# Performance work log

Measured on AMD Instinct MI355X. Metric: run time of the kernel, lower is better.

The kernel has to match this reference:

```python
import jax, jax.numpy as jnp
import numpy as np

B, T, S1, S2 = 64, 256, 256, 256
E = 512   # tgt_word_vec_size
D = 512   # decoder_rnn_size
NT_V, RULE_V = 600, 50000


def _attention(q, ctx, mask, Wa, Wo):
    # OpenNMT GlobalAttention, attn_type='general', no bias.
    # q: [B, D], ctx: [B, S, D], mask: [B, S] bool
    scores = jnp.einsum('bd,bsd->bs', q @ Wa, ctx)
    scores = jnp.where(mask, scores, jnp.float32(-1e9))
    a = jax.nn.softmax(scores, axis=-1)
    c = jnp.einsum('bs,bsd->bd', a, ctx)
    out = jnp.tanh(jnp.concatenate([c, q], axis=-1) @ Wo)
    return out, a


def _lstm_cell(x, h, c, Wih, Whh, b):
    g = x @ Wih.T + h @ Whh.T + b
    i, f, gg, o = jnp.split(g, 4, axis=-1)  # torch gate order i,f,g,o
    c2 = jax.nn.sigmoid(f) * c + jax.nn.sigmoid(i) * jnp.tanh(gg)
    h2 = jax.nn.sigmoid(o) * jnp.tanh(c2)
    return h2, c2


def setup_inputs() -> dict:
    key = jax.random.key(0)
    ks = jax.random.split(key, 20)
    s = 0.02
    inp = {
        'nt': jax.random.randint(ks[0], (B, T), 0, NT_V, dtype=jnp.int32),
        'prev_rules': jax.random.randint(ks[1], (B, T), 0, RULE_V, dtype=jnp.int32),
        'parent_rules': jax.random.randint(ks[2], (B, T), 0, RULE_V, dtype=jnp.int32),
        'parent_idx': jax.random.randint(ks[3], (B, T), 0, T, dtype=jnp.int32),
        'src_context': jax.random.normal(ks[4], (B, S1, D), jnp.float32),
        'rest_context': jax.random.normal(ks[5], (B, S2, D), jnp.float32),
        'src_mask': jnp.ones((B, S1), dtype=bool),
        'rest_mask': jnp.ones((B, S2), dtype=bool),
        'h0': jax.random.normal(ks[6], (B, D), jnp.float32),
        'c0': jax.random.normal(ks[7], (B, D), jnp.float32),
        'nt_emb': jax.random.normal(ks[8], (NT_V, E), jnp.float32) * s,
        'rule_emb': jax.random.normal(ks[9], (RULE_V, E), jnp.float32) * s,
        'Wih': jax.random.normal(ks[10], (4 * D, 3 * E + D), jnp.float32) * s,
        'Whh': jax.random.normal(ks[11], (4 * D, D), jnp.float32) * s,
        'b_lstm': jnp.zeros((4 * D,), jnp.float32),
        'Wa_src': jax.random.normal(ks[12], (D, D), jnp.float32) * s,
        'Wo_src': jax.random.normal(ks[13], (2 * D, D), jnp.float32) * s,
        'Wa_var': jax.random.normal(ks[14], (D, D), jnp.float32) * s,
        'Wo_var': jax.random.normal(ks[15], (2 * D, D), jnp.float32) * s,
        'Wl': jax.random.normal(ks[16], (3 * D, D), jnp.float32) * s,
        'bl': jnp.zeros((D,), jnp.float32),
    }
    return inp


def reference(nt, prev_rules, parent_rules, parent_idx, src_context, rest_context,
              src_mask, rest_mask, h0, c0, nt_emb, rule_emb, Wih, Whh, b_lstm,
              Wa_src, Wo_src, Wa_var, Wo_var, Wl, bl):
    b, t = nt.shape
    d = h0.shape[-1]
    nt_e = nt_emb[nt]              # [B,T,E]
    rule_e = rule_emb[prev_rules]  # [B,T,E]
    prule_e = rule_emb[parent_rules]
    buf0 = jnp.zeros((b, t, d), src_context.dtype)  # rnn_output buffer (tree parent states)

    def step(carry, xs):
        h, c, buf = carry
        nt_t, r_t, pr_t, pidx_t, ti = xs
        # parent state: earlier rnn_output per batch element (zeros if not yet written)
        parent = jnp.take_along_axis(buf, pidx_t[:, None, None], axis=1)[:, 0]  # [B,D]
        x = jnp.concatenate([nt_t, r_t, pr_t, parent], axis=-1)
        h, c = _lstm_cell(x, h, c, Wih, Whh, b_lstm)
        src_out, _ = _attention(h, src_context, src_mask, Wa_src, Wo_src)
        var_out, var_sc = _attention(src_out, rest_context, rest_mask, Wa_var, Wo_var)
        ao = jnp.tanh(jnp.concatenate([h, src_out, var_out], axis=-1) @ Wl + bl)
        buf = jax.lax.dynamic_update_slice_in_dim(buf, h[:, None, :], ti, axis=1)
        return (h, c, buf), (ao, var_sc)

    xs = (nt_e.transpose(1, 0, 2), rule_e.transpose(1, 0, 2), prule_e.transpose(1, 0, 2),
          parent_idx.T, jnp.arange(t))
    _, (outs, scores) = jax.lax.scan(step, (h0, c0, buf0), xs)
    output = outs.transpose(1, 0, 2)       # [B,T,D]
    attn_scores = scores.transpose(1, 0, 2)  # [B,T,S2]
    # forward returns (output, attn_scores, copy_attn_scores); copy == var scores
    return output, attn_scores, attn_scores
```

## Files before the change

kernel.cpp:

```cpp
#include <hip/hip_runtime.h>
#include <hip/hip_bf16.h>
#include <math.h>

typedef __bf16 bf16;
typedef float  f32x4  __attribute__((ext_vector_type(4)));
typedef bf16   bf16x8 __attribute__((ext_vector_type(8)));
typedef bf16   bf16x4 __attribute__((ext_vector_type(4)));
typedef unsigned long long u64;

#define NB 64
#define NT 256
#define NS 256
#define ND 512

__device__ __forceinline__ f32x4 mfma16(bf16x8 a, bf16x8 b, f32x4 c) {
  return __builtin_amdgcn_mfma_f32_16x16x32_bf16(a, b, c, 0, 0, 0);
}

__global__ void k_cast_bt(bf16* dst, int dstStride, int N, int K,
                          const float* src, int srcLd, int srcOff, int transpose) {
  int id = blockIdx.x * 256 + threadIdx.x;
  if (id >= N * K) return;
  int n = id / K, k = id % K;
  float v = transpose ? src[(size_t)k * srcLd + srcOff + n]
                      : src[(size_t)n * srcLd + srcOff + k];
  dst[(size_t)n * dstStride + k] = (bf16)v;
}

__global__ void k_init(const float* h0, bf16* h0bf, unsigned* bar) {
  int id = blockIdx.x * 256 + threadIdx.x;
  if (id < NB * ND) h0bf[id] = (bf16)h0[id];
  if (id == 0) *bar = 0u;
}

__global__ void k_embed(const int* __restrict__ nt, const int* __restrict__ pr,
                        const int* __restrict__ par, const float* __restrict__ nt_emb,
                        const float* __restrict__ rule_emb, bf16* __restrict__ Abuf) {
  int r = blockIdx.x;
  int tid = threadIdx.x;
  const float* s0 = nt_emb  + (size_t)nt[r]  * 512;
  const float* s1 = rule_emb + (size_t)pr[r]  * 512;
  const float* s2 = rule_emb + (size_t)par[r] * 512;
  bf16* drow = Abuf + (size_t)r * 1536;
  for (int v = 0; v < 3; ++v) {
    int col = (tid + v * 128) * 4;
    const float* s = (col < 512) ? (s0 + col) : (col < 1024 ? s1 + col - 512 : s2 + col - 1024);
    float4 x = *(const float4*)s;
    bf16x4 y; y[0] = (bf16)x.x; y[1] = (bf16)x.y; y[2] = (bf16)x.z; y[3] = (bf16)x.w;
    *(bf16x4*)(drow + col) = y;
  }
}

__global__ __launch_bounds__(256) void k_gemm(
    const bf16* __restrict__ A0, int k0, const bf16* __restrict__ A1, int k1,
    const bf16* __restrict__ A2, int k2, const bf16* __restrict__ Bt,
    int Ktot, int N, int nbx, const float* __restrict__ bias, int act,
    float* __restrict__ Cf, bf16* __restrict__ Cbf) {
  __shared__ bf16 Al[128 * 40];
  __shared__ bf16 Bl[128 * 40];
  const int tid = threadIdx.x;
  const int bx = blockIdx.x % nbx, by = blockIdx.x / nbx;
  const int w = tid >> 6, l = tid & 63;
  const int wm = (w & 1) * 64, wn = (w >> 1) * 64;
  const int la = l & 15, kq = (l >> 4) * 8;
  const int srow = tid >> 1, skh = (tid & 1) * 16;
  const int m_g = by * 128 + srow;
  const bf16* brow = Bt + (size_t)(bx * 128 + srow) * Ktot;

  f32x4 acc[4][4];
  f32x4 z; z[0] = 0.f; z[1] = 0.f; z[2] = 0.f; z[3] = 0.f;
#pragma unroll
  for (int mt = 0; mt < 4; ++mt)
#pragma unroll
    for (int nt2 = 0; nt2 < 4; ++nt2) acc[mt][nt2] = z;

  for (int kt = 0; kt < Ktot; kt += 32) {
    __syncthreads();
    {
      int kg = kt + skh;
      const bf16* p;
      int kk = kg;
      if (kk < k0) p = A0 + (size_t)m_g * k0 + kk;
      else { kk -= k0;
        if (kk < k1) p = A1 + (size_t)m_g * k1 + kk;
        else { kk -= k1; p = A2 + (size_t)m_g * k2 + kk; } }
      *(bf16x8*)(&Al[srow * 40 + skh])     = *(const bf16x8*)p;
      *(bf16x8*)(&Al[srow * 40 + skh + 8]) = *(const bf16x8*)(p + 8);
      const bf16* q = brow + kt + skh;
      *(bf16x8*)(&Bl[srow * 40 + skh])     = *(const bf16x8*)q;
      *(bf16x8*)(&Bl[srow * 40 + skh + 8]) = *(const bf16x8*)(q + 8);
    }
    __syncthreads();
    bf16x8 af[4], bfr[4];
#pragma unroll
    for (int mt = 0; mt < 4; ++mt) af[mt]  = *(const bf16x8*)(&Al[(wm + mt * 16 + la) * 40 + kq]);
#pragma unroll
    for (int nt2 = 0; nt2 < 4; ++nt2) bfr[nt2] = *(const bf16x8*)(&Bl[(wn + nt2 * 16 + la) * 40 + kq]);
#pragma unroll
    for (int mt = 0; mt < 4; ++mt)
#pragma unroll
      for (int nt2 = 0; nt2 < 4; ++nt2)
        acc[mt][nt2] = mfma16(af[mt], bfr[nt2], acc[mt][nt2]);
  }
  const int r4 = (l >> 4) * 4, cc = l & 15;
#pragma unroll
  for (int mt = 0; mt < 4; ++mt)
#pragma unroll
    for (int nt2 = 0; nt2 < 4; ++nt2)
#pragma unroll
      for (int i = 0; i < 4; ++i) {
        int mm = by * 128 + wm + mt * 16 + r4 + i;
        int nn = bx * 128 + wn + nt2 * 16 + cc;
        float v = acc[mt][nt2][i];
        if (bias) v += bias[nn];
        if (act) v = tanhf(v);
        size_t off = (size_t)mm * N + nn;
        if (Cf)  Cf[off]  = v;
        if (Cbf) Cbf[off] = (bf16)v;
      }
}

__global__ __launch_bounds__(512, 2) void k_lstm_all(
    const bf16* __restrict__ gpre, const bf16* __restrict__ W2bt,
    const int* __restrict__ parent_idx, const bf16* __restrict__ h0bf,
    const float* __restrict__ c0,
    bf16* __restrict__ Hbf, float* __restrict__ H, unsigned* __restrict__ bar) {
  __shared__ bf16 Als[2][64 * 72];
  __shared__ float gls[64 * 68];
  const int tid = threadIdx.x;
  const int bid = blockIdx.x;
  const int d0 = bid * 16;
  const int w = tid >> 6, l = tid & 63;
  const int wm = (w & 1) * 32;
  const int wn = (w >> 1) * 16;
  const int la16 = l & 15, kq8 = (l >> 4) * 8, r4 = (l >> 4) * 4;
  const int am = tid >> 3;
  const int akoff = (tid & 7) * 8;
  const int pb = tid >> 3, pd = (tid & 7) * 2;

  const int ng = (wn >> 4) * 512 + d0 + la16;
  bf16x8 wf[32];
#pragma unroll
  for (int kc = 0; kc < 32; ++kc)
    wf[kc] = *(const bf16x8*)(W2bt + (size_t)ng * 1024 + kc * 32 + kq8);

  float creg0 = c0[pb * ND + d0 + pd];
  float creg1 = c0[pb * ND + d0 + pd + 1];

  unsigned g_pf[4];
#pragma unroll
  for (int g = 0; g < 4; ++g)
    g_pf[g] = *(const unsigned*)(gpre + ((size_t)pb * NT + 0) * 2048 + g * 512 + d0 + pd);

  for (int t = 0; t < NT; ++t) {
    const int pidx_v = parent_idx[am * NT + t];
    const bool haspar = (pidx_v < t);
    const bf16* hsrc = (t == 0) ? (h0bf + (size_t)am * ND)
                                : (Hbf + ((size_t)am * NT + (t - 1)) * ND);
    const bf16* psrc = Hbf + ((size_t)am * NT + pidx_v) * ND;

    auto issueA = [&](int it, u64& x0, u64& x1) {
      if (it < 8) {
        const bf16* p = hsrc + it * 64 + akoff;
        x0 = __hip_atomic_load((const u64*)p,       __ATOMIC_RELAXED, __HIP_MEMORY_SCOPE_AGENT);
        x1 = __hip_atomic_load((const u64*)(p + 4), __ATOMIC_RELAXED, __HIP_MEMORY_SCOPE_AGENT);
      } else if (haspar) {
        const bf16* p = psrc + (it - 8) * 64 + akoff;
        x0 = __hip_atomic_load((const u64*)p,       __ATOMIC_RELAXED, __HIP_MEMORY_SCOPE_AGENT);
        x1 = __hip_atomic_load((const u64*)(p + 4), __ATOMIC_RELAXED, __HIP_MEMORY_SCOPE_AGENT);
      } else { x0 = 0ull; x1 = 0ull; }
    };
    auto wrA = [&](int buf, u64 x0, u64 x1) {
      *(u64*)(&Als[buf][am * 72 + akoff])     = x0;
      *(u64*)(&Als[buf][am * 72 + akoff + 4]) = x1;
    };

    u64 s0a, s0b, s1a, s1b;
    issueA(0, s0a, s0b);
    issueA(1, s1a, s1b);
    wrA(0, s0a, s0b);
    issueA(2, s0a, s0b);
    __syncthreads();

    f32x4 acc[2];
    f32x4 zf; zf[0] = 0.f; zf[1] = 0.f; zf[2] = 0.f; zf[3] = 0.f;
    acc[0] = zf; acc[1] = zf;

#pragma unroll
    for (int it = 0; it < 16; ++it) {
      const int cur = it & 1, nxt = cur ^ 1;
      if (it < 15) {
        if (nxt) { wrA(1, s1a, s1b); if (it + 3 < 16) issueA(it + 3, s1a, s1b); }
        else     { wrA(0, s0a, s0b); if (it + 3 < 16) issueA(it + 3, s0a, s0b); }
      }
      const bf16* base = Als[cur];
      bf16x8 af[2][2];
#pragma unroll
      for (int mt = 0; mt < 2; ++mt)
#pragma unroll
        for (int kh = 0; kh < 2; ++kh)
          af[mt][kh] = *(const bf16x8*)(base + (wm + mt * 16 + la16) * 72 + kh * 32 + kq8);
#pragma unroll
      for (int mt = 0; mt < 2; ++mt)
#pragma unroll
        for (int kh = 0; kh < 2; ++kh)
          acc[mt] = mfma16(af[mt][kh], wf[2 * it + kh], acc[mt]);
      __syncthreads();
    }

#pragma unroll
    for (int mt = 0; mt < 2; ++mt)
#pragma unroll
      for (int i = 0; i < 4; ++i)
        gls[(wm + mt * 16 + r4 + i) * 68 + wn + la16] = acc[mt][i];
    __syncthreads();

    {
      union { unsigned u; bf16 h[2]; } gv[4];
#pragma unroll
      for (int g = 0; g < 4; ++g) gv[g].u = g_pf[g];
      float hn[2];
#pragma unroll
      for (int j = 0; j < 2; ++j) {
        float gi = gls[pb * 68 +  0 + pd + j] + (float)gv[0].h[j];
        float gf = gls[pb * 68 + 16 + pd + j] + (float)gv[1].h[j];
        float gg = gls[pb * 68 + 32 + pd + j] + (float)gv[2].h[j];
        float go = gls[pb * 68 + 48 + pd + j] + (float)gv[3].h[j];
        float si = 1.f / (1.f + __expf(-gi));
        float sf = 1.f / (1.f + __expf(-gf));
        float so = 1.f / (1.f + __expf(-go));
        float cp = j ? creg1 : creg0;
        float cn = sf * cp + si * tanhf(gg);
        if (j) creg1 = cn; else creg0 = cn;
        hn[j] = so * tanhf(cn);
      }
      size_t hoff = ((size_t)pb * NT + t) * ND + d0 + pd;
      union { unsigned u; bf16 h[2]; } pk;
      pk.h[0] = (bf16)hn[0]; pk.h[1] = (bf16)hn[1];
      __hip_atomic_store((unsigned*)(Hbf + hoff), pk.u, __ATOMIC_RELAXED, __HIP_MEMORY_SCOPE_AGENT);
      *(float2*)(H + hoff) = make_float2(hn[0], hn[1]);
    }

    if (t + 1 < NT) {
#pragma unroll
      for (int g = 0; g < 4; ++g)
        g_pf[g] = *(const unsigned*)(gpre + ((size_t)pb * NT + (t + 1)) * 2048 + g * 512 + d0 + pd);
      __syncthreads();
      if (tid == 0) {
        __hip_atomic_fetch_add(bar, 1u, __ATOMIC_RELAXED, __HIP_MEMORY_SCOPE_AGENT);
        const unsigned target = 32u * (unsigned)(t + 1);
        while (__hip_atomic_load(bar, __ATOMIC_RELAXED, __HIP_MEMORY_SCOPE_AGENT) < target)
          __builtin_amdgcn_s_sleep(1);
      }
      __syncthreads();
    }
  }
}

__global__ __launch_bounds__(256) void k_gemm_f32(
    const float* __restrict__ A, const float* __restrict__ Bm, float* __restrict__ C,
    int M, int N, int K, int nbx) {
  __shared__ float At[16 * 68];
  __shared__ float Bs[16 * 68];
  const int tid = threadIdx.x;
  const int bx = blockIdx.x % nbx, by = blockIdx.x / nbx;
  const int ty = tid >> 4, tx = tid & 15;
  const int am = tid >> 2, ak = (tid & 3) * 4;
  const int bk = tid >> 4, bn = (tid & 15) * 4;
  float acc[4][4] = {};
  for (int kb = 0; kb < K; kb += 16) {
    __syncthreads();
    float4 a4 = *(const float4*)(A + (size_t)(by * 64 + am) * K + kb + ak);
    At[(ak + 0) * 68 + am] = a4.x; At[(ak + 1) * 68 + am] = a4.y;
    At[(ak + 2) * 68 + am] = a4.z; At[(ak + 3) * 68 + am] = a4.w;
    *(float4*)(&Bs[bk * 68 + bn]) = *(const float4*)(Bm + (size_t)(kb + bk) * N + bx * 64 + bn);
    __syncthreads();
#pragma unroll
    for (int kk = 0; kk < 16; ++kk) {
      float4 av = *(const float4*)(&At[kk * 68 + ty * 4]);
      float4 bv = *(const float4*)(&Bs[kk * 68 + tx * 4]);
      float aa[4] = {av.x, av.y, av.z, av.w};
      float bb[4] = {bv.x, bv.y, bv.z, bv.w};
#pragma unroll
      for (int i = 0; i < 4; ++i)
#pragma unroll
        for (int j = 0; j < 4; ++j) acc[i][j] += aa[i] * bb[j];
    }
  }
#pragma unroll
  for (int i = 0; i < 4; ++i) {
    float4 o; o.x = acc[i][0]; o.y = acc[i][1]; o.z = acc[i][2]; o.w = acc[i][3];
    *(float4*)(C + (size_t)(by * 64 + ty * 4 + i) * N + bx * 64 + tx * 4) = o;
  }
}

__global__ __launch_bounds__(256) void k_attn(
    const float* __restrict__ Q, const float* __restrict__ ctx, bf16* __restrict__ Cbf,
    float* __restrict__ prob0, float* __restrict__ prob1) {
  __shared__ float Sl[64 * 257];
  __shared__ float T1[16 * 68];
  __shared__ float T2[16 * 68];
  const int tid = threadIdx.x;
  const int b = blockIdx.x >> 2, ch = blockIdx.x & 3;
  const int t0 = ch * 64;
  const int row0 = b * NT + t0;
  const int ty = tid >> 4, tx = tid & 15;
  const int sl_r = tid >> 2, sl_k = (tid & 3) * 4;

  for (int sc = 0; sc < 4; ++sc) {
    float acc[4][4] = {};
    for (int kc = 0; kc < 512; kc += 16) {
      __syncthreads();
      float4 q4 = *(const float4*)(Q + (size_t)(row0 + sl_r) * ND + kc + sl_k);
      T1[(sl_k + 0) * 68 + sl_r] = q4.x; T1[(sl_k + 1) * 68 + sl_r] = q4.y;
      T1[(sl_k + 2) * 68 + sl_r] = q4.z; T1[(sl_k + 3) * 68 + sl_r] = q4.w;
      float4 c4 = *(const float4*)(ctx + (size_t)(b * NS + sc * 64 + sl_r) * ND + kc + sl_k);
      T2[(sl_k + 0) * 68 + sl_r] = c4.x; T2[(sl_k + 1) * 68 + sl_r] = c4.y;
      T2[(sl_k + 2) * 68 + sl_r] = c4.z; T2[(sl_k + 3) * 68 + sl_r] = c4.w;
      __syncthreads();
#pragma unroll
      for (int kk = 0; kk < 16; ++kk) {
        float4 qv = *(const float4*)(&T1[kk * 68 + ty * 4]);
        float4 cv = *(const float4*)(&T2[kk * 68 + tx * 4]);
        float qa[4] = {qv.x, qv.y, qv.z, qv.w};
        float ca[4] = {cv.x, cv.y, cv.z, cv.w};
#pragma unroll
        for (int i = 0; i < 4; ++i)
#pragma unroll
          for (int j = 0; j < 4; ++j) acc[i][j] += qa[i] * ca[j];
      }
    }
#pragma unroll
    for (int i = 0; i < 4; ++i)
#pragma unroll
      for (int j = 0; j < 4; ++j)
        Sl[(ty * 4 + i) * 257 + sc * 64 + tx * 4 + j] = acc[i][j];
  }
  __syncthreads();

  if (tid < 64) {
    float* row = &Sl[tid * 257];
    float mx = -1e30f;
    for (int s = 0; s < 256; ++s) mx = fmaxf(mx, row[s]);
    float sum = 0.f;
    for (int s = 0; s < 256; ++s) { float e = __expf(row[s] - mx); row[s] = e; sum += e; }
    float inv = 1.f / sum;
    for (int s = 0; s < 256; ++s) row[s] *= inv;
  }
  __syncthreads();
  if (prob0) {
    int pr = tid >> 2, pq = (tid & 3) * 64;
    size_t po = (size_t)(row0 + pr) * NS + pq;
    for (int s = 0; s < 64; s += 4) {
      float4 o; o.x = Sl[pr * 257 + pq + s];     o.y = Sl[pr * 257 + pq + s + 1];
      o.z = Sl[pr * 257 + pq + s + 2];           o.w = Sl[pr * 257 + pq + s + 3];
      *(float4*)(prob0 + po + s) = o;
      *(float4*)(prob1 + po + s) = o;
    }
  }

  const int c_sr = tid >> 4, c_n4 = (tid & 15) * 4;
  for (int dc = 0; dc < 512; dc += 64) {
    float acc[4][4] = {};
    for (int s0c = 0; s0c < 256; s0c += 16) {
      __syncthreads();
      *(float4*)(&T2[c_sr * 68 + c_n4]) =
          *(const float4*)(ctx + (size_t)(b * NS + s0c + c_sr) * ND + dc + c_n4);
      __syncthreads();
#pragma unroll
      for (int kk = 0; kk < 16; ++kk) {
        float p0 = Sl[(ty * 4 + 0) * 257 + s0c + kk];
        float p1 = Sl[(ty * 4 + 1) * 257 + s0c + kk];
        float p2 = Sl[(ty * 4 + 2) * 257 + s0c + kk];
        float p3 = Sl[(ty * 4 + 3) * 257 + s0c + kk];
        float4 cv = *(const float4*)(&T2[kk * 68 + tx * 4]);
        float ca[4] = {cv.x, cv.y, cv.z, cv.w};
#pragma unroll
        for (int j = 0; j < 4; ++j) {
          acc[0][j] += p0 * ca[j]; acc[1][j] += p1 * ca[j];
          acc[2][j] += p2 * ca[j]; acc[3][j] += p3 * ca[j];
        }
      }
    }
#pragma unroll
    for (int i = 0; i < 4; ++i)
#pragma unroll
      for (int j = 0; j < 4; ++j)
        Cbf[(size_t)(row0 + ty * 4 + i) * ND + dc + tx * 4 + j] = (bf16)acc[i][j];
  }
}

extern "C" void kernel_launch(void* const* d_in, const int* in_sizes, int n_in,
                              void* d_out, int out_size, void* d_ws, size_t ws_size,
                              hipStream_t stream) {
  const int*   nt       = (const int*)d_in[0];
  const int*   prules   = (const int*)d_in[1];
  const int*   parules  = (const int*)d_in[2];
  const int*   pidx     = (const int*)d_in[3];
  const float* src_ctx  = (const float*)d_in[4];
  const float* rest_ctx = (const float*)d_in[5];
  const float* h0       = (const float*)d_in[8];
  const float* c0       = (const float*)d_in[9];
  const float* nt_emb   = (const float*)d_in[10];
  const float* rule_emb = (const float*)d_in[11];
  const float* Wih      = (const float*)d_in[12];
  const float* Whh      = (const float*)d_in[13];
  const float* b_lstm   = (const float*)d_in[14];
  const float* Wa_src   = (const float*)d_in[15];
  const float* Wo_src   = (const float*)d_in[16];
  const float* Wa_var   = (const float*)d_in[17];
  const float* Wo_var   = (const float*)d_in[18];
  const float* Wl       = (const float*)d_in[19];
  const float* bl       = (const float*)d_in[20];
  float* out = (float*)d_out;

  char* p = (char*)d_ws;
  bf16*  Abuf    = (bf16*)p;  p += 50331648;
  bf16*  gpre    = (bf16*)p;  p += 67108864;
  float* H       = (float*)p; p += 33554432;
  bf16*  Hbf     = (bf16*)p;  p += 16777216;
  float* SRCOUT  = (float*)p; p += 33554432;
  bf16*  SRCOUTb = (bf16*)p;  p += 16777216;
  bf16*  Wemb_bt = (bf16*)p;  p += 6291456;
  bf16*  W2bt    = (bf16*)p;  p += 4194304;
  bf16*  Wos_bt  = (bf16*)p;  p += 1048576;
  bf16*  Wov_bt  = (bf16*)p;  p += 1048576;
  bf16*  Wl_bt   = (bf16*)p;  p += 1572864;
  bf16*  h0bf    = (bf16*)p;  p += 65536;
  unsigned* bar  = (unsigned*)p; p += 256;
  float* Q1    = (float*)Abuf;
  bf16*  C1bf  = (bf16*)((char*)Abuf + 33554432);
  float* Q2    = (float*)gpre;
  bf16*  C2bf  = (bf16*)((char*)gpre + 33554432);
  bf16*  VARbf = (bf16*)((char*)gpre + 50331648);
  float* out_p0 = out + 8388608;
  float* out_p1 = out + 12582912;

  k_cast_bt<<<(2048*1536+255)/256, 256, 0, stream>>>(Wemb_bt, 1536, 2048, 1536, Wih, 2048, 0, 0);
  k_cast_bt<<<(2048*512 +255)/256, 256, 0, stream>>>(W2bt,        1024, 2048, 512, Whh, 512, 0, 0);
  k_cast_bt<<<(2048*512 +255)/256, 256, 0, stream>>>(W2bt + 512,  1024, 2048, 512, Wih, 2048, 1536, 0);
  k_cast_bt<<<(512*1024 +255)/256, 256, 0, stream>>>(Wos_bt, 1024, 512, 1024, Wo_src, 512, 0, 1);
  k_cast_bt<<<(512*1024 +255)/256, 256, 0, stream>>>(Wov_bt, 1024, 512, 1024, Wo_var, 512, 0, 1);
  k_cast_bt<<<(512*1536 +255)/256, 256, 0, stream>>>(Wl_bt,  1536, 512, 1536, Wl, 512, 0, 1);
  k_init<<<128, 256, 0, stream>>>(h0, h0bf, bar);
  k_embed<<<16384, 128, 0, stream>>>(nt, prules, parules, nt_emb, rule_emb, Abuf);

  k_gemm<<<2048, 256, 0, stream>>>(Abuf, 1536, nullptr, 0, nullptr, 0,
                                   Wemb_bt, 1536, 2048, 16, b_lstm, 0, nullptr, gpre);

  k_lstm_all<<<32, 512, 0, stream>>>(gpre, W2bt, pidx, h0bf, c0, Hbf, H, bar);

  k_gemm_f32<<<2048, 256, 0, stream>>>(H, Wa_src, Q1, 16384, 512, 512, 8);
  k_attn<<<256, 256, 0, stream>>>(Q1, src_ctx, C1bf, nullptr, nullptr);
  k_gemm<<<512, 256, 0, stream>>>(C1bf, 512, Hbf, 512, nullptr, 0,
                                  Wos_bt, 1024, 512, 4, nullptr, 1, SRCOUT, SRCOUTb);
  k_gemm_f32<<<2048, 256, 0, stream>>>(SRCOUT, Wa_var, Q2, 16384, 512, 512, 8);
  k_attn<<<256, 256, 0, stream>>>(Q2, rest_ctx, C2bf, out_p0, out_p1);
  k_gemm<<<512, 256, 0, stream>>>(C2bf, 512, SRCOUTb, 512, nullptr, 0,
                                  Wov_bt, 1024, 512, 4, nullptr, 1, nullptr, VARbf);
  k_gemm<<<512, 256, 0, stream>>>(Hbf, 512, SRCOUTb, 512, VARbf, 512,
                                  Wl_bt, 1536, 512, 4, bl, 1, out, nullptr);
}
```

Baseline: 3.168 ms.

## Restructure persistent LSTM recurrence with split-batch blocks, flag barrier and early parent GEMM

The recurrent LSTM kernel now runs 64 blocks, each handling half the batch for 16 hidden units. Warps are split so half compute the h-part of the recurrent GEMM with 32x32 MFMAs while the other half prefetch the parent state and compute the parent contribution ahead of the grid barrier, unless a parent is the just-produced step, in which case it is deferred. The single atomic counter barrier is replaced by per-block flags polled by one wavefront. Hidden states are also written to a time-major buffer so the next step loads them contiguously into LDS. This aims to shorten the serial per-step critical path, at the cost of more LDS, a second store per step, and more complex synchronisation.

```diff
diff --git a/kernel.cpp b/kernel.cpp
--- a/kernel.cpp
+++ b/kernel.cpp
@@ -4,6 +4,7 @@
 
 typedef __bf16 bf16;
 typedef float  f32x4  __attribute__((ext_vector_type(4)));
+typedef float  f32x16 __attribute__((ext_vector_type(16)));
 typedef bf16   bf16x8 __attribute__((ext_vector_type(8)));
 typedef bf16   bf16x4 __attribute__((ext_vector_type(4)));
 typedef unsigned long long u64;
@@ -15,6 +16,9 @@
 
 __device__ __forceinline__ f32x4 mfma16(bf16x8 a, bf16x8 b, f32x4 c) {
   return __builtin_amdgcn_mfma_f32_16x16x32_bf16(a, b, c, 0, 0, 0);
+}
+__device__ __forceinline__ f32x16 mfma32(bf16x8 a, bf16x8 b, f32x16 c) {
+  return __builtin_amdgcn_mfma_f32_32x32x16_bf16(a, b, c, 0, 0, 0);
 }
 
 __global__ void k_cast_bt(bf16* dst, int dstStride, int N, int K,
@@ -30,7 +34,7 @@
 __global__ void k_init(const float* h0, bf16* h0bf, unsigned* bar) {
   int id = blockIdx.x * 256 + threadIdx.x;
   if (id < NB * ND) h0bf[id] = (bf16)h0[id];
-  if (id == 0) *bar = 0u;
+  if (id < 1024) bar[id] = 0u;
 }
 
 __global__ void k_embed(const int* __restrict__ nt, const int* __restrict__ pr,
@@ -120,140 +124,194 @@
       }
 }
 
+#define LSTM_LDS 100992
+
 __global__ __launch_bounds__(512, 2) void k_lstm_all(
     const bf16* __restrict__ gpre, const bf16* __restrict__ W2bt,
     const int* __restrict__ parent_idx, const bf16* __restrict__ h0bf,
     const float* __restrict__ c0,
-    bf16* __restrict__ Hbf, float* __restrict__ H, unsigned* __restrict__ bar) {
-  __shared__ bf16 Als[2][64 * 72];
-  __shared__ float gls[64 * 68];
+    bf16* __restrict__ Hbf,
+    bf16* __restrict__ Ht,
+    float* __restrict__ H, unsigned* __restrict__ flags) {
+  extern __shared__ char smem[];
+  bf16*  Als      = (bf16*)smem;
+  float* gls      = (float*)(smem + 66048);
+  unsigned* latew = (unsigned*)(smem + 100864);
+
   const int tid = threadIdx.x;
   const int bid = blockIdx.x;
-  const int d0 = bid * 16;
+  const int bg = bid & 1, cg = bid >> 1;
+  const int d0 = cg * 16;
   const int w = tid >> 6, l = tid & 63;
-  const int wm = (w & 1) * 32;
-  const int wn = (w >> 1) * 16;
-  const int la16 = l & 15, kq8 = (l >> 4) * 8, r4 = (l >> 4) * 4;
-  const int am = tid >> 3;
-  const int akoff = (tid & 7) * 8;
-  const int pb = tid >> 3, pd = (tid & 7) * 2;
-
-  const int ng = (wn >> 4) * 512 + d0 + la16;
-  bf16x8 wf[32];
-#pragma unroll
-  for (int kc = 0; kc < 32; ++kc)
-    wf[kc] = *(const bf16x8*)(W2bt + (size_t)ng * 1024 + kc * 32 + kq8);
-
-  float creg0 = c0[pb * ND + d0 + pd];
-  float creg1 = c0[pb * ND + d0 + pd + 1];
-
+  const int la32 = l & 31, lhi = l >> 5, kq8 = lhi * 8;
+  const int n2 = w & 1, kq = w >> 1;
+  const int lc = n2 * 32 + la32;
+  const int ng = (lc >> 4) * 512 + d0 + (lc & 15);
+
+  bf16x8 wf[16];
+#pragma unroll
+  for (int kc = 0; kc < 16; ++kc)
+    wf[kc] = *(const bf16x8*)(W2bt + (size_t)ng * 1024 + kq * 256 + kc * 16 + kq8);
+
+  const int pb = (tid & 255) >> 3;
+  const int pdh = (tid & 7) * 2;
+  const int gb = bg * 32 + pb;
+  const int ss = tid & 255, pr = ss & 31, po = ss >> 5;
+  const int pgb = bg * 32 + pr;
+
+  float creg0 = 0.f, creg1 = 0.f;
   unsigned g_pf[4];
-#pragma unroll
-  for (int g = 0; g < 4; ++g)
-    g_pf[g] = *(const unsigned*)(gpre + ((size_t)pb * NT + 0) * 2048 + g * 512 + d0 + pd);
+  if (tid < 256) {
+    creg0 = c0[(size_t)gb * ND + d0 + pdh];
+    creg1 = c0[(size_t)gb * ND + d0 + pdh + 1];
+#pragma unroll
+    for (int g = 0; g < 4; ++g)
+      g_pf[g] = *(const unsigned*)(gpre + ((size_t)gb * NT) * 2048 + g * 512 + d0 + pdh);
+  }
+
+  if (w < 4) {
+    const bf16* src = h0bf + (size_t)bg * 32 * ND;
+#pragma unroll
+    for (int j = 0; j < 16; ++j) {
+      u64 x = *(const u64*)(src + w * 4096 + j * 256 + l * 4);
+      *(u64*)(&Als[(w * 8 + (j >> 1)) * 1032 + (j & 1) * 256 + l * 4]) = x;
+    }
+  }
+  f32x16 acc;
+#pragma unroll
+  for (int i = 0; i < 16; ++i) acc[i] = 0.f;
+  bool deferred = false;
+  __syncthreads();
 
   for (int t = 0; t < NT; ++t) {
-    const int pidx_v = parent_idx[am * NT + t];
-    const bool haspar = (pidx_v < t);
-    const bf16* hsrc = (t == 0) ? (h0bf + (size_t)am * ND)
-                                : (Hbf + ((size_t)am * NT + (t - 1)) * ND);
-    const bf16* psrc = Hbf + ((size_t)am * NT + pidx_v) * ND;
-
-    auto issueA = [&](int it, u64& x0, u64& x1) {
-      if (it < 8) {
-        const bf16* p = hsrc + it * 64 + akoff;
-        x0 = __hip_atomic_load((const u64*)p,       __ATOMIC_RELAXED, __HIP_MEMORY_SCOPE_AGENT);
-        x1 = __hip_atomic_load((const u64*)(p + 4), __ATOMIC_RELAXED, __HIP_MEMORY_SCOPE_AGENT);
-      } else if (haspar) {
-        const bf16* p = psrc + (it - 8) * 64 + akoff;
-        x0 = __hip_atomic_load((const u64*)p,       __ATOMIC_RELAXED, __HIP_MEMORY_SCOPE_AGENT);
-        x1 = __hip_atomic_load((const u64*)(p + 4), __ATOMIC_RELAXED, __HIP_MEMORY_SCOPE_AGENT);
-      } else { x0 = 0ull; x1 = 0ull; }
-    };
-    auto wrA = [&](int buf, u64 x0, u64 x1) {
-      *(u64*)(&Als[buf][am * 72 + akoff])     = x0;
-      *(u64*)(&Als[buf][am * 72 + akoff + 4]) = x1;
-    };
-
-    u64 s0a, s0b, s1a, s1b;
-    issueA(0, s0a, s0b);
-    issueA(1, s1a, s1b);
-    wrA(0, s0a, s0b);
-    issueA(2, s0a, s0b);
-    __syncthreads();
-
-    f32x4 acc[2];
-    f32x4 zf; zf[0] = 0.f; zf[1] = 0.f; zf[2] = 0.f; zf[3] = 0.f;
-    acc[0] = zf; acc[1] = zf;
-
-#pragma unroll
-    for (int it = 0; it < 16; ++it) {
-      const int cur = it & 1, nxt = cur ^ 1;
-      if (it < 15) {
-        if (nxt) { wrA(1, s1a, s1b); if (it + 3 < 16) issueA(it + 3, s1a, s1b); }
-        else     { wrA(0, s0a, s0b); if (it + 3 < 16) issueA(it + 3, s0a, s0b); }
-      }
-      const bf16* base = Als[cur];
-      bf16x8 af[2][2];
-#pragma unroll
-      for (int mt = 0; mt < 2; ++mt)
-#pragma unroll
-        for (int kh = 0; kh < 2; ++kh)
-          af[mt][kh] = *(const bf16x8*)(base + (wm + mt * 16 + la16) * 72 + kh * 32 + kq8);
-#pragma unroll
-      for (int mt = 0; mt < 2; ++mt)
-#pragma unroll
-        for (int kh = 0; kh < 2; ++kh)
-          acc[mt] = mfma16(af[mt][kh], wf[2 * it + kh], acc[mt]);
-      __syncthreads();
-    }
-
-#pragma unroll
-    for (int mt = 0; mt < 2; ++mt)
-#pragma unroll
-      for (int i = 0; i < 4; ++i)
-        gls[(wm + mt * 16 + r4 + i) * 68 + wn + la16] = acc[mt][i];
-    __syncthreads();
-
-    {
+    u64 preg[16];
+    if (w < 4) {
+#pragma unroll
+      for (int kc = 0; kc < 16; ++kc) {
+        bf16x8 a = *(const bf16x8*)(&Als[la32 * 1032 + kq * 256 + kc * 16 + kq8]);
+        acc = mfma32(a, wf[kc], acc);
+      }
+    } else {
+      if (deferred) {
+#pragma unroll
+        for (int kc = 0; kc < 16; ++kc) {
+          bf16x8 a = *(const bf16x8*)(&Als[la32 * 1032 + kq * 256 + kc * 16 + kq8]);
+          acc = mfma32(a, wf[kc], acc);
+        }
+      }
+      if (t + 1 < NT) {
+        int pv = parent_idx[(size_t)pgb * NT + t + 1];
+        if (pv < t) {
+          const bf16* p = Hbf + ((size_t)pgb * NT + pv) * ND + po * 64;
+#pragma unroll
+          for (int j = 0; j < 16; ++j)
+            preg[j] = __hip_atomic_load((const u64*)(p + j * 4),
+                                        __ATOMIC_RELAXED, __HIP_MEMORY_SCOPE_AGENT);
+        } else {
+#pragma unroll
+          for (int j = 0; j < 16; ++j) preg[j] = 0ull;
+        }
+      }
+    }
+#pragma unroll
+    for (int i = 0; i < 16; ++i) {
+      int row = (i & 3) + 8 * (i >> 2) + 4 * lhi;
+      gls[(kq * 32 + row) * 68 + lc] = acc[i];
+    }
+#pragma unroll
+    for (int i = 0; i < 16; ++i) acc[i] = 0.f;
+    __syncthreads();
+
+    if (tid < 256) {
       union { unsigned u; bf16 h[2]; } gv[4];
 #pragma unroll
       for (int g = 0; g < 4; ++g) gv[g].u = g_pf[g];
       float hn[2];
 #pragma unroll
       for (int j = 0; j < 2; ++j) {
-        float gi = gls[pb * 68 +  0 + pd + j] + (float)gv[0].h[j];
-        float gf = gls[pb * 68 + 16 + pd + j] + (float)gv[1].h[j];
-        float gg = gls[pb * 68 + 32 + pd + j] + (float)gv[2].h[j];
-        float go = gls[pb * 68 + 48 + pd + j] + (float)gv[3].h[j];
-        float si = 1.f / (1.f + __expf(-gi));
-        float sf = 1.f / (1.f + __expf(-gf));
-        float so = 1.f / (1.f + __expf(-go));
+        float s[4];
+#pragma unroll
+        for (int g = 0; g < 4; ++g) {
+          float v = 0.f;
+#pragma unroll
+          for (int q = 0; q < 4; ++q) v += gls[(q * 32 + pb) * 68 + g * 16 + pdh + j];
+          s[g] = v + (float)gv[g].h[j];
+        }
+        float si = 1.f / (1.f + __expf(-s[0]));
+        float sf = 1.f / (1.f + __expf(-s[1]));
+        float so = 1.f / (1.f + __expf(-s[3]));
+        float e2 = __expf(2.f * fminf(fmaxf(s[2], -15.f), 15.f));
+        float tg = (e2 - 1.f) / (e2 + 1.f);
         float cp = j ? creg1 : creg0;
-        float cn = sf * cp + si * tanhf(gg);
+        float cn = sf * cp + si * tg;
+        float e2c = __expf(2.f * fminf(fmaxf(cn, -15.f), 15.f));
+        float tc = (e2c - 1.f) / (e2c + 1.f);
         if (j) creg1 = cn; else creg0 = cn;
-        hn[j] = so * tanhf(cn);
-      }
-      size_t hoff = ((size_t)pb * NT + t) * ND + d0 + pd;
+        hn[j] = so * tc;
+      }
       union { unsigned u; bf16 h[2]; } pk;
       pk.h[0] = (bf16)hn[0]; pk.h[1] = (bf16)hn[1];
-      __hip_atomic_store((unsigned*)(Hbf + hoff), pk.u, __ATOMIC_RELAXED, __HIP_MEMORY_SCOPE_AGENT);
-      *(float2*)(H + hoff) = make_float2(hn[0], hn[1]);
-    }
-
-    if (t + 1 < NT) {
-#pragma unroll
-      for (int g = 0; g < 4; ++g)
-        g_pf[g] = *(const unsigned*)(gpre + ((size_t)pb * NT + (t + 1)) * 2048 + g * 512 + d0 + pd);
-      __syncthreads();
-      if (tid == 0) {
-        __hip_atomic_fetch_add(bar, 1u, __ATOMIC_RELAXED, __HIP_MEMORY_SCOPE_AGENT);
-        const unsigned target = 32u * (unsigned)(t + 1);
-        while (__hip_atomic_load(bar, __ATOMIC_RELAXED, __HIP_MEMORY_SCOPE_AGENT) < target)
-          __builtin_amdgcn_s_sleep(1);
-      }
-      __syncthreads();
-    }
+      size_t hb = ((size_t)gb * NT + t) * ND + d0 + pdh;
+      size_t ho = ((size_t)t * NB + gb) * ND + d0 + pdh;
+      __hip_atomic_store((unsigned*)(Hbf + hb), pk.u, __ATOMIC_RELAXED, __HIP_MEMORY_SCOPE_AGENT);
+      __hip_atomic_store((unsigned*)(Ht + ho), pk.u, __ATOMIC_RELAXED, __HIP_MEMORY_SCOPE_AGENT);
+      *(float2*)(H + hb) = make_float2(hn[0], hn[1]);
+      if (t + 1 < NT) {
+#pragma unroll
+        for (int g = 0; g < 4; ++g)
+          g_pf[g] = *(const unsigned*)(gpre + ((size_t)gb * NT + t + 1) * 2048 + g * 512 + d0 + pdh);
+      }
+    }
+
+    bool deferred_next = false;
+    if (w >= 4 && t + 1 < NT) {
+#pragma unroll
+      for (int j = 0; j < 16; ++j)
+        *(u64*)(&Als[pr * 1032 + 512 + po * 64 + j * 4]) = preg[j];
+      int pv2 = parent_idx[(size_t)(bg * 32 + la32) * NT + t + 1];
+      unsigned mask = (unsigned)__ballot(pv2 == t);
+      if (tid == 256) *latew = mask;
+      deferred_next = (mask != 0u);
+    }
+    if (t + 1 == NT) break;
+    __syncthreads();
+
+    if (w == 0) {
+      if (l == 0)
+        __hip_atomic_store(flags + bid * 16, (unsigned)(t + 1),
+                           __ATOMIC_RELAXED, __HIP_MEMORY_SCOPE_AGENT);
+      const unsigned tgt = (unsigned)(t + 1);
+      const unsigned* fp = flags + l * 16;
+      while (!__all((int)(__hip_atomic_load(fp, __ATOMIC_RELAXED,
+                                            __HIP_MEMORY_SCOPE_AGENT) >= tgt)))
+        __builtin_amdgcn_s_sleep(1);
+    } else if (w >= 4 && !deferred_next) {
+#pragma unroll
+      for (int kc = 0; kc < 16; ++kc) {
+        bf16x8 a = *(const bf16x8*)(&Als[la32 * 1032 + kq * 256 + kc * 16 + kq8]);
+        acc = mfma32(a, wf[kc], acc);
+      }
+    }
+    __syncthreads();
+
+    if (w < 4) {
+      unsigned lmask = *latew;
+      const bf16* src = Ht + ((size_t)t * NB + bg * 32) * ND;
+      u64 hreg[16];
+#pragma unroll
+      for (int j = 0; j < 16; ++j)
+        hreg[j] = __hip_atomic_load((const u64*)(src + w * 4096 + j * 256 + l * 4),
+                                    __ATOMIC_RELAXED, __HIP_MEMORY_SCOPE_AGENT);
+#pragma unroll
+      for (int j = 0; j < 16; ++j) {
+        const int row = w * 8 + (j >> 1), col = (j & 1) * 256 + l * 4;
+        *(u64*)(&Als[row * 1032 + col]) = hreg[j];
+        if ((lmask >> row) & 1u)
+          *(u64*)(&Als[row * 1032 + 512 + col]) = hreg[j];
+      }
+    }
+    __syncthreads();
+    deferred = deferred_next;
   }
 }
 
@@ -427,7 +485,8 @@
   bf16*  Wov_bt  = (bf16*)p;  p += 1048576;
   bf16*  Wl_bt   = (bf16*)p;  p += 1572864;
   bf16*  h0bf    = (bf16*)p;  p += 65536;
-  unsigned* bar  = (unsigned*)p; p += 256;
+  unsigned* bar  = (unsigned*)p; p += 4096;
+  bf16*  Ht    = (bf16*)Abuf;
   float* Q1    = (float*)Abuf;
   bf16*  C1bf  = (bf16*)((char*)Abuf + 33554432);
   float* Q2    = (float*)gpre;
@@ -435,6 +494,9 @@
   bf16*  VARbf = (bf16*)((char*)gpre + 50331648);
   float* out_p0 = out + 8388608;
   float* out_p1 = out + 12582912;
+
+  hipFuncSetAttribute(reinterpret_cast<const void*>(k_lstm_all),
+                      hipFuncAttributeMaxDynamicSharedMemorySize, LSTM_LDS);
 
   k_cast_bt<<<(2048*1536+255)/256, 256, 0, stream>>>(Wemb_bt, 1536, 2048, 1536, Wih, 2048, 0, 0);
   k_cast_bt<<<(2048*512 +255)/256, 256, 0, stream>>>(W2bt,        1024, 2048, 512, Whh, 512, 0, 0);
@@ -448,7 +510,7 @@
   k_gemm<<<2048, 256, 0, stream>>>(Abuf, 1536, nullptr, 0, nullptr, 0,
                                    Wemb_bt, 1536, 2048, 16, b_lstm, 0, nullptr, gpre);
 
-  k_lstm_all<<<32, 512, 0, stream>>>(gpre, W2bt, pidx, h0bf, c0, Hbf, H, bar);
+  k_lstm_all<<<64, 512, LSTM_LDS, stream>>>(gpre, W2bt, pidx, h0bf, c0, Hbf, Ht, H, bar);
 
   k_gemm_f32<<<2048, 256, 0, stream>>>(H, Wa_src, Q1, 16384, 512, 512, 8);
   k_attn<<<256, 256, 0, stream>>>(Q1, src_ctx, C1bf, nullptr, nullptr);
```

Result: faster. 2.601 ms (-17.9%).
